# Performance work log

Hardware: AMD Instinct MI355X
Metric: run time of the kernel (lower is better)

## Reference

```python
import jax, jax.numpy as jnp
import numpy as np
from jax import lax

# Boundary-condition copy pairs on the 18x18 zero-padded lattice: padded[dst] = padded[src].
# Verified against the torch source: no src is overwritten before being read, so one gather suffices.
_DST = np.array([(1,3),(1,5),(2,7),(3,9),(4,10),(4,11),(6,13),(7,13),(8,14),(10,15),(11,15),(12,16),
                 (14,15),(14,16),(15,15),(16,14),(17,13),(17,11),(16,9),(15,7),(14,6),(14,5),(12,3),
                 (10,2),(8,1),(6,0),(4,0),(4,1),(3,1),(2,2),(5,0),(9,2),(13,4),(15,8),(17,12),(15,14),(13,16)])
_SRC = np.array([(13,15),(13,5),(14,7),(15,9),(16,10),(16,11),(6,1),(7,1),(8,2),(10,3),(11,3),(12,4),
                 (2,3),(2,4),(3,3),(4,2),(5,1),(5,11),(4,9),(3,7),(2,6),(2,5),(12,15),(10,14),(8,13),
                 (6,12),(16,12),(16,13),(15,13),(14,14),(5,12),(9,14),(1,4),(3,8),(5,12),(3,2),(1,4)])

def _make_mask():
    m = np.ones((16, 16), np.float32)
    for i in range(8):
        m[i, 8 + i:16] = 0
    for i in range(7):
        m[9 + i, :i + 1] = 0
    m[0, 4:8] = 0; m[1, 6:9] = 0; m[2, 8:10] = 0; m[3, 9:11] = 0
    m[5, 12] = 0; m[6, 12:14] = 0; m[7, 13:15] = 0; m[8, 14:16] = 0
    m[9, 14:16] = 0; m[10, 14:16] = 0; m[11, 15] = 0; m[12, 15] = 0
    m[13:, 14:] = 0; m[14, 13] = 0; m[15, 13] = 0; m[15, 7:9] = 0
    m[13, 5] = 0; m[14, 6:8] = 0; m[8, 0:2] = 0; m[9, 1] = 0
    m[7, 0] = 0; m[3, 0] = 0; m[0:3, 0] = 0; m[0:2, 0:2] = 0; m[0, 2] = 0
    return m

_MASK = jnp.asarray(_make_mask())  # [16,16]

def setup_inputs() -> dict:
    key = jax.random.key(0)
    kx, kw, kb = jax.random.split(key, 3)
    B, Cin, Cout = 2048, 128, 128
    x = jax.random.normal(kx, (B, Cin, 16, 16), dtype=jnp.float32)
    W = jax.random.normal(kw, (Cout, Cin, 3, 3), dtype=jnp.float32) * (1.0 / np.sqrt(Cin * 9))
    b = jax.random.normal(kb, (Cout,), dtype=jnp.float32) * 0.01
    return {"x": x, "W": W, "b": b}

def reference(x, W, b):
    # zero-pad 16x16 -> 18x18
    xp = jnp.pad(x, ((0, 0), (0, 0), (1, 1), (1, 1)))
    dr = jnp.asarray(_DST[:, 0]); dc = jnp.asarray(_DST[:, 1])
    sr = jnp.asarray(_SRC[:, 0]); sc = jnp.asarray(_SRC[:, 1])
    # fused boundary-condition gather (replaces 37 tiny copies)
    xp = xp.at[:, :, dr, dc].set(xp[:, :, sr, sc])
    out = lax.conv_general_dilated(
        xp, W, window_strides=(1, 1), padding='VALID',
        dimension_numbers=('NCHW', 'OIHW', 'NCHW'))  # [B,Cout,16,16]
    out = out + b[None, :, None, None]
    # fused zero-masking epilogue (replaces ~40 tiny zeroing writes)
    return out * _MASK
```

## Files before the change

### kernel.cpp

```cpp
#include <hip/hip_runtime.h>


typedef _Float16 f16x8 __attribute__((ext_vector_type(8)));
typedef float    f32x4 __attribute__((ext_vector_type(4)));
typedef unsigned short u16x8 __attribute__((ext_vector_type(8)));

#define ROW_BYTES      256
#define ZERO_ROW       256
#define X_BYTES        65792
#define MASK_OFF       65792
#define BIAS_OFF       66816
#define MAP_OFF        67328
#define SMEM_BYTES     67976

#define W_FRAG_ELEMS   147456

#define BCP(a,b,c,d) ((unsigned)((a)<<24)|((b)<<16)|((c)<<8)|(d))
__constant__ unsigned int BC_PAIRS[37] = {
    BCP(1,3,13,15),  BCP(1,5,13,5),   BCP(2,7,14,7),   BCP(3,9,15,9),
    BCP(4,10,16,10), BCP(4,11,16,11), BCP(6,13,6,1),   BCP(7,13,7,1),
    BCP(8,14,8,2),   BCP(10,15,10,3), BCP(11,15,11,3), BCP(12,16,12,4),
    BCP(14,15,2,3),  BCP(14,16,2,4),  BCP(15,15,3,3),  BCP(16,14,4,2),
    BCP(17,13,5,1),  BCP(17,11,5,11), BCP(16,9,4,9),   BCP(15,7,3,7),
    BCP(14,6,2,6),   BCP(14,5,2,5),   BCP(12,3,12,15), BCP(10,2,10,14),
    BCP(8,1,8,13),   BCP(6,0,6,12),   BCP(4,0,16,12),  BCP(4,1,16,13),
    BCP(3,1,15,13),  BCP(2,2,14,14),  BCP(5,0,5,12),   BCP(9,2,9,14),
    BCP(13,4,1,4),   BCP(15,8,3,8),   BCP(17,12,5,12), BCP(15,14,3,2),
    BCP(13,16,1,4)
};

__device__ __forceinline__ bool mask_zero(int r, int c) {
    bool z = false;
    z |= (r < 8 && c >= 8 + r);
    z |= (r >= 9 && c <= r - 9);
    z |= (r == 0 && c >= 4 && c < 8);
    z |= (r == 1 && c >= 6 && c < 9);
    z |= (r == 2 && (c == 8 || c == 9));
    z |= (r == 3 && (c == 9 || c == 10));
    z |= (r == 5 && c == 12);
    z |= (r == 6 && (c == 12 || c == 13));
    z |= (r == 7 && (c == 13 || c == 14));
    z |= (r == 8 && (c == 14 || c == 15));
    z |= (r == 9 && (c == 14 || c == 15));
    z |= (r == 10 && (c == 14 || c == 15));
    z |= (r == 11 && c == 15);
    z |= (r == 12 && c == 15);
    z |= (r >= 13 && c >= 14);
    z |= (r == 14 && c == 13);
    z |= (r == 15 && c == 13);
    z |= (r == 15 && (c == 7 || c == 8));
    z |= (r == 13 && c == 5);
    z |= (r == 14 && (c == 6 || c == 7));
    z |= (r == 8 && (c == 0 || c == 1));
    z |= (r == 9 && c == 1);
    z |= (r == 7 && c == 0);
    z |= (r == 3 && c == 0);
    z |= (r <= 2 && c == 0);
    z |= (r <= 1 && c <= 1);
    z |= (r == 0 && c == 2);
    return z;
}

__global__ void kag_prep_w(const float* __restrict__ W, _Float16* __restrict__ wf) {
    int g  = blockIdx.x * 256 + threadIdx.x;
    int j  = g & 7;
    int l  = (g >> 3) & 63;
    int ct = (g >> 9) & 7;
    int it = g >> 12;
    int t  = it >> 2;
    int ks = it & 3;
    int co = ct * 16 + (l & 15);
    int ci = ks * 32 + ((l >> 4) & 3) * 8 + j;
    wf[g] = (_Float16)W[(co * 128 + ci) * 9 + t];
}

__global__ __launch_bounds__(512, 4) void kag_main(
    const float* __restrict__ x, const float* __restrict__ bias,
    const _Float16* __restrict__ wf, float* __restrict__ out)
{
    extern __shared__ char smem[];
    const int tid = threadIdx.x;
    const int b   = blockIdx.x;
    const float* xb = x + (size_t)b * 32768;

    {
        int p       = tid & 255;
        int halfsel = tid >> 8;
        int px      = p & 15;
        char* rowbase = smem + p * ROW_BYTES;
        #pragma unroll
        for (int g = 0; g < 8; ++g) {
            int ci0 = halfsel * 64 + g * 8;
            f16x8 hv;
            #pragma unroll
            for (int j = 0; j < 8; ++j)
                hv[j] = (_Float16)xb[(size_t)(ci0 + j) * 256 + p];
            int slot = (ci0 >> 3) ^ px;
            *(f16x8*)(rowbase + (slot << 4)) = hv;
        }
    }
    if (tid < 16) {
        u16x8 z = (u16x8)0;
        *(u16x8*)(smem + ZERO_ROW * ROW_BYTES + tid * 16) = z;
    }
    if (tid < 256) {
        int r = tid >> 4, c = tid & 15;
        ((float*)(smem + MASK_OFF))[tid] = mask_zero(r, c) ? 0.0f : 1.0f;
    }
    if (tid < 128) ((float*)(smem + BIAS_OFF))[tid] = bias[tid];
    for (int i = tid; i < 324; i += 512) {
        int r = i / 18, c = i - r * 18;
        unsigned short v = ZERO_ROW;
        if (r >= 1 && r <= 16 && c >= 1 && c <= 16) v = (unsigned short)((r - 1) * 16 + (c - 1));
        ((unsigned short*)(smem + MAP_OFF))[i] = v;
    }
    __syncthreads();
    if (tid < 37) {
        unsigned v = BC_PAIRS[tid];
        int dr = v >> 24, dc = (v >> 16) & 255, sr = (v >> 8) & 255, sc = v & 255;
        ((unsigned short*)(smem + MAP_OFF))[dr * 18 + dc] =
            (unsigned short)((sr - 1) * 16 + (sc - 1));
    }
    __syncthreads();

    const int lane   = tid & 63;
    const int w      = tid >> 6;
    const int kg     = (lane >> 4) & 3;
    const int c16    = lane & 15;
    const int ptbase = (w & 3) * 4;
    const int ctbase = (w >> 2) * 4;

    f32x4 acc[16];
    #pragma unroll
    for (int i = 0; i < 16; ++i) acc[i] = (f32x4)0.0f;

    const char* wbase = (const char*)wf + (size_t)ctbase * 1024 + (size_t)lane * 16;
    const unsigned short* mp = (const unsigned short*)(smem + MAP_OFF);

    int kh = 0, kw2 = 0;
    for (int t = 0; t < 9; ++t) {
        int rb[4], rxs[4];
        #pragma unroll
        for (int pp = 0; pp < 4; ++pp) {
            int srow = mp[(ptbase + pp + kh) * 18 + (c16 + kw2)];
            rb[pp]  = srow << 8;
            rxs[pp] = srow & 15;
        }
        #pragma unroll
        for (int ks = 0; ks < 4; ++ks) {
            const char* pf = wbase + (size_t)(t * 4 + ks) * 8192;
            f16x8 A[4];
            #pragma unroll
            for (int c = 0; c < 4; ++c)
                A[c] = *(const f16x8*)(pf + c * 1024);
            f16x8 Bv[4];
            #pragma unroll
            for (int p = 0; p < 4; ++p) {
                int slot = (ks * 4 + kg) ^ rxs[p];
                Bv[p] = *(const f16x8*)(smem + rb[p] + (slot << 4));
            }
            #pragma unroll
            for (int c = 0; c < 4; ++c) {
                #pragma unroll
                for (int p = 0; p < 4; ++p)
                    acc[c * 4 + p] = __builtin_amdgcn_mfma_f32_16x16x32_f16(
                        A[c], Bv[p], acc[c * 4 + p], 0, 0, 0);
            }
        }
        kw2++; if (kw2 == 3) { kw2 = 0; kh++; }
    }

    const float* mk = (const float*)(smem + MASK_OFF);
    const float* bs = (const float*)(smem + BIAS_OFF);
    float* outb = out + (size_t)b * 32768;
    #pragma unroll
    for (int c = 0; c < 4; ++c) {
        int co0 = (ctbase + c) * 16 + kg * 4;
        float b0 = bs[co0], b1 = bs[co0 + 1], b2 = bs[co0 + 2], b3 = bs[co0 + 3];
        #pragma unroll
        for (int p = 0; p < 4; ++p) {
            int pout = (ptbase + p) * 16 + c16;
            float m  = mk[pout];
            f32x4 a  = acc[c * 4 + p];
            float* op = outb + (size_t)co0 * 256 + pout;
            op[0]   = (a[0] + b0) * m;
            op[256] = (a[1] + b1) * m;
            op[512] = (a[2] + b2) * m;
            op[768] = (a[3] + b3) * m;
        }
    }
}

extern "C" void kernel_launch(void* const* d_in, const int* in_sizes, int n_in,
                              void* d_out, int out_size, void* d_ws, size_t ws_size,
                              hipStream_t stream) {
    const float* x    = (const float*)d_in[0];
    const float* W    = (const float*)d_in[1];
    const float* bias = (const float*)d_in[2];
    float* out = (float*)d_out;
    _Float16* wf = (_Float16*)d_ws;

    hipFuncSetAttribute((const void*)kag_main,
                        hipFuncAttributeMaxDynamicSharedMemorySize, SMEM_BYTES);

    kag_prep_w<<<576, 256, 0, stream>>>(W, wf);
    kag_main<<<2048, 512, SMEM_BYTES, stream>>>(x, bias, wf, out);
}
```

Before: 513.9 us.

## Switch to 32x32x16 MFMA with software-pipelined weight and LDS operand loads

New measurement: 536.3 us. 1.04x slower.

```diff
diff --git a/kernel.cpp b/kernel.cpp
--- a/kernel.cpp
+++ b/kernel.cpp
@@ -2,18 +2,15 @@
 
 
 typedef _Float16 f16x8 __attribute__((ext_vector_type(8)));
-typedef float    f32x4 __attribute__((ext_vector_type(4)));
+typedef float    f32x16 __attribute__((ext_vector_type(16)));
 typedef unsigned short u16x8 __attribute__((ext_vector_type(8)));
 
 #define ROW_BYTES      256
 #define ZERO_ROW       256
-#define X_BYTES        65792
 #define MASK_OFF       65792
 #define BIAS_OFF       66816
 #define MAP_OFF        67328
 #define SMEM_BYTES     67976
-
-#define W_FRAG_ELEMS   147456
 
 #define BCP(a,b,c,d) ((unsigned)((a)<<24)|((b)<<16)|((c)<<8)|(d))
 __constant__ unsigned int BC_PAIRS[37] = {
@@ -65,14 +62,39 @@
     int g  = blockIdx.x * 256 + threadIdx.x;
     int j  = g & 7;
     int l  = (g >> 3) & 63;
-    int ct = (g >> 9) & 7;
-    int it = g >> 12;
-    int t  = it >> 2;
-    int ks = it & 3;
-    int co = ct * 16 + (l & 15);
-    int ci = ks * 32 + ((l >> 4) & 3) * 8 + j;
-    wf[g] = (_Float16)W[(co * 128 + ci) * 9 + t];
-}
+    int ct = (g >> 9) & 3;
+    int it = g >> 11;
+    int tap = it >> 3;
+    int ks  = it & 7;
+    int co = ct * 32 + (l & 31);
+    int ci = ks * 16 + ((l >> 5) & 1) * 8 + j;
+    wf[g] = (_Float16)W[(co * 128 + ci) * 9 + tap];
+}
+
+#define MFMA32(A, B, C) __builtin_amdgcn_mfma_f32_32x32x16_f16(A, B, C, 0, 0, 0)
+
+#define STEP(LOC, S3, S2, RB0, RB1) do {                                        \
+    acc00 = MFMA32(A##S3##c0, B##S2##p0, acc00);                                \
+    acc01 = MFMA32(A##S3##c0, B##S2##p1, acc01);                                \
+    acc10 = MFMA32(A##S3##c1, B##S2##p0, acc10);                                \
+    acc11 = MFMA32(A##S3##c1, B##S2##p1, acc11);                                \
+    { int it3_ = t3*8 + (LOC) + 3; it3_ = it3_ > 71 ? 71 : it3_;                \
+      const char* pw_ = wb + it3_ * 4096;                                       \
+      A##S3##c0 = *(const f16x8*)pw_;                                           \
+      A##S3##c1 = *(const f16x8*)(pw_ + 1024); }                                \
+    { const int ks2_ = ((LOC) + 2) & 7;                                         \
+      B##S2##p0 = *(const f16x8*)(smem + (RB0) +                                \
+          ((((ks2_ * 2) + half) ^ (((RB0) >> 8) & 15)) << 4));                  \
+      B##S2##p1 = *(const f16x8*)(smem + (RB1) +                                \
+          ((((ks2_ * 2) + half) ^ (((RB1) >> 8) & 15)) << 4)); }                \
+} while (0)
+
+#define LOADMAP(TAP, R0, R1) do {                                               \
+    int t_ = (TAP); t_ = t_ > 8 ? 8 : t_;                                       \
+    int kh_ = (t_ * 11) >> 5; int kw_ = t_ - kh_ * 3;                           \
+    R0 = ((int)mp[(prow0 + kh_) * 18 + pcol + kw_]) << 8;                       \
+    R1 = ((int)mp[(prow1 + kh_) * 18 + pcol + kw_]) << 8;                       \
+} while (0)
 
 __global__ __launch_bounds__(512, 4) void kag_main(
     const float* __restrict__ x, const float* __restrict__ bias,
@@ -123,72 +145,76 @@
     }
     __syncthreads();
 
-    const int lane   = tid & 63;
-    const int w      = tid >> 6;
-    const int kg     = (lane >> 4) & 3;
-    const int c16    = lane & 15;
-    const int ptbase = (w & 3) * 4;
-    const int ctbase = (w >> 2) * 4;
-
-    f32x4 acc[16];
-    #pragma unroll
-    for (int i = 0; i < 16; ++i) acc[i] = (f32x4)0.0f;
-
-    const char* wbase = (const char*)wf + (size_t)ctbase * 1024 + (size_t)lane * 16;
+    const int lane = tid & 63;
+    const int w    = tid >> 6;
+    const int l31  = lane & 31;
+    const int half = lane >> 5;
+    const int pt32base = (w & 3) * 2;
+    const int ct32base = (w >> 2) * 2;
+
+    const int prow0 = (pt32base + 0) * 2 + (l31 >> 4);
+    const int prow1 = (pt32base + 1) * 2 + (l31 >> 4);
+    const int pcol  = lane & 15;
+
     const unsigned short* mp = (const unsigned short*)(smem + MAP_OFF);
-
-    int kh = 0, kw2 = 0;
-    for (int t = 0; t < 9; ++t) {
-        int rb[4], rxs[4];
-        #pragma unroll
-        for (int pp = 0; pp < 4; ++pp) {
-            int srow = mp[(ptbase + pp + kh) * 18 + (c16 + kw2)];
-            rb[pp]  = srow << 8;
-            rxs[pp] = srow & 15;
-        }
-        #pragma unroll
-        for (int ks = 0; ks < 4; ++ks) {
-            const char* pf = wbase + (size_t)(t * 4 + ks) * 8192;
-            f16x8 A[4];
-            #pragma unroll
-            for (int c = 0; c < 4; ++c)
-                A[c] = *(const f16x8*)(pf + c * 1024);
-            f16x8 Bv[4];
-            #pragma unroll
-            for (int p = 0; p < 4; ++p) {
-                int slot = (ks * 4 + kg) ^ rxs[p];
-                Bv[p] = *(const f16x8*)(smem + rb[p] + (slot << 4));
-            }
-            #pragma unroll
-            for (int c = 0; c < 4; ++c) {
-                #pragma unroll
-                for (int p = 0; p < 4; ++p)
-                    acc[c * 4 + p] = __builtin_amdgcn_mfma_f32_16x16x32_f16(
-                        A[c], Bv[p], acc[c * 4 + p], 0, 0, 0);
-            }
-        }
-        kw2++; if (kw2 == 3) { kw2 = 0; kh++; }
+    const char* wb = (const char*)wf + ct32base * 1024 + lane * 16;
+
+    f32x16 acc00 = (f32x16)0.0f, acc01 = (f32x16)0.0f;
+    f32x16 acc10 = (f32x16)0.0f, acc11 = (f32x16)0.0f;
+
+    int m0rb0, m0rb1, m1rb0, m1rb1, m2rb0, m2rb1, m3rb0, m3rb1;
+    LOADMAP(0, m0rb0, m0rb1);
+
+    f16x8 A0c0 = *(const f16x8*)(wb);
+    f16x8 A0c1 = *(const f16x8*)(wb + 1024);
+    f16x8 A1c0 = *(const f16x8*)(wb + 4096);
+    f16x8 A1c1 = *(const f16x8*)(wb + 4096 + 1024);
+    f16x8 A2c0 = *(const f16x8*)(wb + 8192);
+    f16x8 A2c1 = *(const f16x8*)(wb + 8192 + 1024);
+    f16x8 B0p0 = *(const f16x8*)(smem + m0rb0 + (((0 + half) ^ ((m0rb0 >> 8) & 15)) << 4));
+    f16x8 B0p1 = *(const f16x8*)(smem + m0rb1 + (((0 + half) ^ ((m0rb1 >> 8) & 15)) << 4));
+    f16x8 B1p0 = *(const f16x8*)(smem + m0rb0 + (((2 + half) ^ ((m0rb0 >> 8) & 15)) << 4));
+    f16x8 B1p1 = *(const f16x8*)(smem + m0rb1 + (((2 + half) ^ ((m0rb1 >> 8) & 15)) << 4));
+
+    for (int t3 = 0; t3 < 9; t3 += 3) {
+        LOADMAP(t3 + 1, m1rb0, m1rb1);
+        STEP( 0, 0, 0, m0rb0, m0rb1);  STEP( 1, 1, 1, m0rb0, m0rb1);
+        STEP( 2, 2, 0, m0rb0, m0rb1);  STEP( 3, 0, 1, m0rb0, m0rb1);
+        STEP( 4, 1, 0, m0rb0, m0rb1);  STEP( 5, 2, 1, m0rb0, m0rb1);
+        STEP( 6, 0, 0, m1rb0, m1rb1);  STEP( 7, 1, 1, m1rb0, m1rb1);
+        STEP( 8, 2, 0, m1rb0, m1rb1);  STEP( 9, 0, 1, m1rb0, m1rb1);
+        STEP(10, 1, 0, m1rb0, m1rb1);  STEP(11, 2, 1, m1rb0, m1rb1);
+        LOADMAP(t3 + 2, m2rb0, m2rb1);
+        STEP(12, 0, 0, m1rb0, m1rb1);  STEP(13, 1, 1, m1rb0, m1rb1);
+        STEP(14, 2, 0, m2rb0, m2rb1);  STEP(15, 0, 1, m2rb0, m2rb1);
+        STEP(16, 1, 0, m2rb0, m2rb1);  STEP(17, 2, 1, m2rb0, m2rb1);
+        STEP(18, 0, 0, m2rb0, m2rb1);  STEP(19, 1, 1, m2rb0, m2rb1);
+        LOADMAP(t3 + 3, m3rb0, m3rb1);
+        STEP(20, 2, 0, m2rb0, m2rb1);  STEP(21, 0, 1, m2rb0, m2rb1);
+        STEP(22, 1, 0, m3rb0, m3rb1);  STEP(23, 2, 1, m3rb0, m3rb1);
+        m0rb0 = m3rb0; m0rb1 = m3rb1;
     }
 
     const float* mk = (const float*)(smem + MASK_OFF);
     const float* bs = (const float*)(smem + BIAS_OFF);
     float* outb = out + (size_t)b * 32768;
-    #pragma unroll
-    for (int c = 0; c < 4; ++c) {
-        int co0 = (ctbase + c) * 16 + kg * 4;
-        float b0 = bs[co0], b1 = bs[co0 + 1], b2 = bs[co0 + 2], b3 = bs[co0 + 3];
-        #pragma unroll
-        for (int p = 0; p < 4; ++p) {
-            int pout = (ptbase + p) * 16 + c16;
-            float m  = mk[pout];
-            f32x4 a  = acc[c * 4 + p];
-            float* op = outb + (size_t)co0 * 256 + pout;
-            op[0]   = (a[0] + b0) * m;
-            op[256] = (a[1] + b1) * m;
-            op[512] = (a[2] + b2) * m;
-            op[768] = (a[3] + b3) * m;
-        }
-    }
+
+#define STORE(ACC, C2, P2) do {                                                 \
+        int pos_ = (pt32base + (P2)) * 32 + l31;                                \
+        float m_ = mk[pos_];                                                    \
+        int cb_  = (ct32base + (C2)) * 32 + 4 * half;                           \
+        _Pragma("unroll")                                                       \
+        for (int r_ = 0; r_ < 16; ++r_) {                                       \
+            int co_ = cb_ + (r_ & 3) + 8 * (r_ >> 2);                           \
+            outb[(size_t)co_ * 256 + pos_] = (ACC[r_] + bs[co_]) * m_;          \
+        }                                                                       \
+    } while (0)
+
+    STORE(acc00, 0, 0);
+    STORE(acc01, 0, 1);
+    STORE(acc10, 1, 0);
+    STORE(acc11, 1, 1);
+#undef STORE
 }
 
 extern "C" void kernel_launch(void* const* d_in, const int* in_sizes, int n_in,
```
